# Optimization experiments

Hardware: AMD Instinct MI355X
Metric: run time of the kernel (lower is better)

The kernel has to match this reference:

```python
import jax, jax.numpy as jnp
import numpy as np


def setup_inputs() -> dict:
    key = jax.random.key(0)
    ks = jax.random.split(key, 5)
    B, S, D, F = 4, 2048, 1024, 4096
    scale_w1 = 1.0 / np.sqrt(D)
    scale_w2 = 1.0 / np.sqrt(F)
    return {
        "hidden_states": jax.random.normal(ks[0], (B, S, D), dtype=jnp.float32),
        "W1": jax.random.normal(ks[1], (F, D), dtype=jnp.float32) * scale_w1,
        "b1": jax.random.normal(ks[2], (F,), dtype=jnp.float32) * 0.02,
        "W2": jax.random.normal(ks[3], (D, F), dtype=jnp.float32) * scale_w2,
        "b2": jax.random.normal(ks[4], (D,), dtype=jnp.float32) * 0.02,
    }


def _sigmoid_poly(h):
    # cubic polynomial sigmoid approximation: 0.5 + 0.25*h - 0.0208*h^3
    h2 = h * h
    h3 = h2 * h
    return 0.5 + 0.25 * h + (-0.0208) * h3


def reference(hidden_states, W1, b1, W2, b2):
    # secure linear projection == plain affine: x @ W.T + b
    h = jnp.einsum("bsd,fd->bsf", hidden_states, W1) + b1  # [B,S,F]
    sw = h * _sigmoid_poly(h)                               # swish via poly sigmoid
    out = jnp.einsum("bsf,df->bsd", sw, W2) + b2            # [B,S,D]
    return out
```

## Files before the change

kernel.cpp:

```cpp
#include <hip/hip_runtime.h>
#include <hip/hip_bf16.h>

typedef __bf16 bf16_t;
typedef __bf16 bf16x8 __attribute__((ext_vector_type(8)));
typedef float f32x16 __attribute__((ext_vector_type(16)));

__global__ __launch_bounds__(256) void cast3_f32_to_bf16(
    const float* __restrict__ a, bf16_t* __restrict__ ao, int na8,
    const float* __restrict__ b, bf16_t* __restrict__ bo, int nb8,
    const float* __restrict__ c, bf16_t* __restrict__ co, int nc8) {
  int i = blockIdx.x * blockDim.x + threadIdx.x;
  const float* in;
  bf16_t* out;
  int j;
  if (i < na8) {
    in = a; out = ao; j = i;
  } else if (i < na8 + nb8) {
    in = b; out = bo; j = i - na8;
  } else if (i < na8 + nb8 + nc8) {
    in = c; out = co; j = i - na8 - nb8;
  } else {
    return;
  }
  const float4* in4 = (const float4*)in;
  float4 f0 = in4[2 * j];
  float4 f1 = in4[2 * j + 1];
  bf16x8 o;
  o[0] = (bf16_t)f0.x; o[1] = (bf16_t)f0.y;
  o[2] = (bf16_t)f0.z; o[3] = (bf16_t)f0.w;
  o[4] = (bf16_t)f1.x; o[5] = (bf16_t)f1.y;
  o[6] = (bf16_t)f1.z; o[7] = (bf16_t)f1.w;
  ((bf16x8*)out)[j] = o;
}

__device__ __forceinline__ void gload_lds16(const bf16_t* g, bf16_t* l) {
  __builtin_amdgcn_global_load_lds(
      (const __attribute__((address_space(1))) void*)g,
      (__attribute__((address_space(3))) void*)l,
      16, 0, 0);
}

template <bool SWISH>
__global__ __launch_bounds__(256, 2) void gemm_bt(
    const bf16_t* __restrict__ A, const bf16_t* __restrict__ B,
    const float* __restrict__ bias, void* __restrict__ Cout,
    int M, int N, int K, int XW, int px, int py) {
  const int tid = threadIdx.x;
  const int wave = tid >> 6;
  const int lane = tid & 63;

  const int bid = blockIdx.x;
  const int xcd = bid & 7;
  const int idx = bid >> 3;
  const int cx = xcd % XW;
  const int cy = xcd / XW;
  const int bx = cx * px + idx % px;
  const int by = cy * py + idx / px;
  const int tileM = by << 8;
  const int tileN = bx << 7;

  __shared__ __align__(16) bf16_t sA[256 * 64];
  __shared__ __align__(16) bf16_t sB[128 * 64];

  const int lrow = lane >> 3;
  const int gch = ((lane & 7) ^ lrow) << 3;
  const bf16_t* gA = A + (size_t)(tileM + (wave << 6) + lrow) * K + gch;
  const bf16_t* gB = B + (size_t)(tileN + (wave << 5) + lrow) * K + gch;
  bf16_t* lA = sA + (size_t)(wave << 6) * 64;
  bf16_t* lB = sB + (size_t)(wave << 5) * 64;

  const int wr = wave >> 1, wc = wave & 1;
  const int frow = lane & 31;
  const int p0 = (((lane >> 5) ^ (lane & 7)) << 3);
  int offA[4], offB[2];
#pragma unroll
  for (int i = 0; i < 4; ++i)
    offA[i] = (wr * 128 + i * 32 + frow) * 64 + p0;
#pragma unroll
  for (int j = 0; j < 2; ++j)
    offB[j] = (wc * 64 + j * 32 + frow) * 64 + p0;

  f32x16 acc[4][2] = {};

  for (int kt = 0; kt < K; kt += 64) {
#pragma unroll
    for (int r = 0; r < 8; ++r)
      gload_lds16(gA + kt + (size_t)(r * 8) * K, lA + r * 8 * 64);
#pragma unroll
    for (int r = 0; r < 4; ++r)
      gload_lds16(gB + kt + (size_t)(r * 8) * K, lB + r * 8 * 64);
    __syncthreads();

#pragma unroll
    for (int s = 0; s < 4; ++s) {
      const int sx = s << 4;
      bf16x8 af[4], bg[2];
#pragma unroll
      for (int i = 0; i < 4; ++i)
        af[i] = *(const bf16x8*)(sA + (offA[i] ^ sx));
#pragma unroll
      for (int j = 0; j < 2; ++j)
        bg[j] = *(const bf16x8*)(sB + (offB[j] ^ sx));
#pragma unroll
      for (int i = 0; i < 4; ++i)
#pragma unroll
        for (int j = 0; j < 2; ++j)
          acc[i][j] = __builtin_amdgcn_mfma_f32_32x32x16_bf16(
              af[i], bg[j], acc[i][j], 0, 0, 0);
    }
    __syncthreads();
  }

  const int halfsel = (lane >> 5) << 2;
#pragma unroll
  for (int i = 0; i < 4; ++i) {
    const int row0 = tileM + wr * 128 + i * 32 + halfsel;
#pragma unroll
    for (int j = 0; j < 2; ++j) {
      const int col = tileN + wc * 64 + j * 32 + (lane & 31);
      const float bv = bias[col];
#pragma unroll
      for (int r = 0; r < 16; ++r) {
        const int row = row0 + (r & 3) + ((r >> 2) << 3);
        float h = acc[i][j][r] + bv;
        if constexpr (SWISH) {
          float h3 = h * h * h;
          float sw = h * (0.5f + 0.25f * h - 0.0208f * h3);
          ((bf16_t*)Cout)[(size_t)row * N + col] = (bf16_t)sw;
        } else {
          ((float*)Cout)[(size_t)row * N + col] = h;
        }
      }
    }
  }
}

extern "C" void kernel_launch(void* const* d_in, const int* in_sizes, int n_in,
                              void* d_out, int out_size, void* d_ws,
                              size_t ws_size, hipStream_t stream) {
  const float* X  = (const float*)d_in[0];
  const float* W1 = (const float*)d_in[1];
  const float* b1 = (const float*)d_in[2];
  const float* W2 = (const float*)d_in[3];
  const float* b2 = (const float*)d_in[4];
  float* out = (float*)d_out;

  const int F = in_sizes[2];
  const int D = in_sizes[4];
  const int M = in_sizes[0] / D;

  bf16_t* Xb  = (bf16_t*)d_ws;
  bf16_t* W1b = Xb + (size_t)M * D;
  bf16_t* W2b = W1b + (size_t)F * D;
  bf16_t* SW  = W2b + (size_t)D * F;

  const int nX = (M * D) / 8, nW1 = (F * D) / 8, nW2 = (D * F) / 8;
  const int nTot = nX + nW1 + nW2;
  cast3_f32_to_bf16<<<(nTot + 255) / 256, 256, 0, stream>>>(
      X, Xb, nX, W1, W1b, nW1, W2, W2b, nW2);

  {
    const int gx = F / 128, gy = M / 256;
    const int XW = 2, XH = 4;
    const int px = gx / XW, py = gy / XH;
    gemm_bt<true><<<gx * gy, 256, 0, stream>>>(
        Xb, W1b, b1, (void*)SW, M, F, D, XW, px, py);
  }

  {
    const int gx = D / 128, gy = M / 256;
    const int XW = 1, XH = 8;
    const int px = gx / XW, py = gy / XH;
    gemm_bt<false><<<gx * gy, 256, 0, stream>>>(
        SW, W2b, b2, (void*)out, M, D, F, XW, px, py);
  }
}
```

Before: 272.0 us.

## Shrink GEMM tile to 128x128 and prefetch next K-tile via registers

Replaces direct global-to-LDS loads with register-staged loads that fetch the next K-slice while MFMAs run on the current one, then write it to LDS after a barrier. The M tile shrinks from 256 to 128, halving the accumulators per wave and doubling the grid. The aim is to hide global load latency and raise occupancy. The cost is extra VGPRs for staging, an extra barrier per iteration, and lower data reuse per tile, which raises global and L2 traffic.

Measured after the change: 268.4 us. No clear change (-1.3%).

```diff
diff --git a/kernel.cpp b/kernel.cpp
--- a/kernel.cpp
+++ b/kernel.cpp
@@ -33,13 +33,6 @@
   ((bf16x8*)out)[j] = o;
 }
 
-__device__ __forceinline__ void gload_lds16(const bf16_t* g, bf16_t* l) {
-  __builtin_amdgcn_global_load_lds(
-      (const __attribute__((address_space(1))) void*)g,
-      (__attribute__((address_space(3))) void*)l,
-      16, 0, 0);
-}
-
 template <bool SWISH>
 __global__ __launch_bounds__(256, 2) void gemm_bt(
     const bf16_t* __restrict__ A, const bf16_t* __restrict__ B,
@@ -56,65 +49,83 @@
   const int cy = xcd / XW;
   const int bx = cx * px + idx % px;
   const int by = cy * py + idx / px;
-  const int tileM = by << 8;
+  const int tileM = by << 7;
   const int tileN = bx << 7;
 
-  __shared__ __align__(16) bf16_t sA[256 * 64];
+  __shared__ __align__(16) bf16_t sA[128 * 64];
   __shared__ __align__(16) bf16_t sB[128 * 64];
 
   const int lrow = lane >> 3;
   const int gch = ((lane & 7) ^ lrow) << 3;
-  const bf16_t* gA = A + (size_t)(tileM + (wave << 6) + lrow) * K + gch;
+  const bf16_t* gA = A + (size_t)(tileM + (wave << 5) + lrow) * K + gch;
   const bf16_t* gB = B + (size_t)(tileN + (wave << 5) + lrow) * K + gch;
-  bf16_t* lA = sA + (size_t)(wave << 6) * 64;
-  bf16_t* lB = sB + (size_t)(wave << 5) * 64;
+  bf16_t* wAp = sA + (size_t)(wave << 5) * 64 + (lane << 3);
+  bf16_t* wBp = sB + (size_t)(wave << 5) * 64 + (lane << 3);
 
   const int wr = wave >> 1, wc = wave & 1;
   const int frow = lane & 31;
   const int p0 = (((lane >> 5) ^ (lane & 7)) << 3);
-  int offA[4], offB[2];
+  int offA[2], offB[2];
 #pragma unroll
-  for (int i = 0; i < 4; ++i)
-    offA[i] = (wr * 128 + i * 32 + frow) * 64 + p0;
+  for (int i = 0; i < 2; ++i)
+    offA[i] = (wr * 64 + i * 32 + frow) * 64 + p0;
 #pragma unroll
   for (int j = 0; j < 2; ++j)
     offB[j] = (wc * 64 + j * 32 + frow) * 64 + p0;
 
-  f32x16 acc[4][2] = {};
+  f32x16 acc[2][2] = {};
 
-  for (int kt = 0; kt < K; kt += 64) {
+  const int niter = K >> 6;
+
+  bf16x8 vA[4], vB[4];
 #pragma unroll
-    for (int r = 0; r < 8; ++r)
-      gload_lds16(gA + kt + (size_t)(r * 8) * K, lA + r * 8 * 64);
+  for (int r = 0; r < 4; ++r) {
+    vA[r] = *(const bf16x8*)(gA + (size_t)(r * 8) * K);
+    vB[r] = *(const bf16x8*)(gB + (size_t)(r * 8) * K);
+  }
 #pragma unroll
-    for (int r = 0; r < 4; ++r)
-      gload_lds16(gB + kt + (size_t)(r * 8) * K, lB + r * 8 * 64);
-    __syncthreads();
+  for (int r = 0; r < 4; ++r) {
+    *(bf16x8*)(wAp + r * 512) = vA[r];
+    *(bf16x8*)(wBp + r * 512) = vB[r];
+  }
+  __syncthreads();
 
+  for (int it = 0; it < niter; ++it) {
+    if (it + 1 < niter) {
+      const int kt = (it + 1) << 6;
+#pragma unroll
+      for (int r = 0; r < 4; ++r) {
+        vA[r] = *(const bf16x8*)(gA + kt + (size_t)(r * 8) * K);
+        vB[r] = *(const bf16x8*)(gB + kt + (size_t)(r * 8) * K);
+      }
+    }
 #pragma unroll
     for (int s = 0; s < 4; ++s) {
       const int sx = s << 4;
-      bf16x8 af[4], bg[2];
+      bf16x8 a0 = *(const bf16x8*)(sA + (offA[0] ^ sx));
+      bf16x8 a1 = *(const bf16x8*)(sA + (offA[1] ^ sx));
+      bf16x8 b0 = *(const bf16x8*)(sB + (offB[0] ^ sx));
+      bf16x8 b1 = *(const bf16x8*)(sB + (offB[1] ^ sx));
+      acc[0][0] = __builtin_amdgcn_mfma_f32_32x32x16_bf16(a0, b0, acc[0][0], 0, 0, 0);
+      acc[0][1] = __builtin_amdgcn_mfma_f32_32x32x16_bf16(a0, b1, acc[0][1], 0, 0, 0);
+      acc[1][0] = __builtin_amdgcn_mfma_f32_32x32x16_bf16(a1, b0, acc[1][0], 0, 0, 0);
+      acc[1][1] = __builtin_amdgcn_mfma_f32_32x32x16_bf16(a1, b1, acc[1][1], 0, 0, 0);
+    }
+    __syncthreads();
+    if (it + 1 < niter) {
 #pragma unroll
-      for (int i = 0; i < 4; ++i)
-        af[i] = *(const bf16x8*)(sA + (offA[i] ^ sx));
-#pragma unroll
-      for (int j = 0; j < 2; ++j)
-        bg[j] = *(const bf16x8*)(sB + (offB[j] ^ sx));
-#pragma unroll
-      for (int i = 0; i < 4; ++i)
-#pragma unroll
-        for (int j = 0; j < 2; ++j)
-          acc[i][j] = __builtin_amdgcn_mfma_f32_32x32x16_bf16(
-              af[i], bg[j], acc[i][j], 0, 0, 0);
+      for (int r = 0; r < 4; ++r) {
+        *(bf16x8*)(wAp + r * 512) = vA[r];
+        *(bf16x8*)(wBp + r * 512) = vB[r];
+      }
     }
     __syncthreads();
   }
 
   const int halfsel = (lane >> 5) << 2;
 #pragma unroll
-  for (int i = 0; i < 4; ++i) {
-    const int row0 = tileM + wr * 128 + i * 32 + halfsel;
+  for (int i = 0; i < 2; ++i) {
+    const int row0 = tileM + wr * 64 + i * 32 + halfsel;
 #pragma unroll
     for (int j = 0; j < 2; ++j) {
       const int col = tileN + wc * 64 + j * 32 + (lane & 31);
@@ -160,7 +171,7 @@
       X, Xb, nX, W1, W1b, nW1, W2, W2b, nW2);
 
   {
-    const int gx = F / 128, gy = M / 256;
+    const int gx = F / 128, gy = M / 128;
     const int XW = 2, XH = 4;
     const int px = gx / XW, py = gy / XH;
     gemm_bt<true><<<gx * gy, 256, 0, stream>>>(
@@ -168,7 +179,7 @@
   }
 
   {
-    const int gx = D / 128, gy = M / 256;
+    const int gx = D / 128, gy = M / 128;
     const int XW = 1, XH = 8;
     const int px = gx / XW, py = gy / XH;
     gemm_bt<false><<<gx * gy, 256, 0, stream>>>(
```

## Double-buffer GEMM tiles via register staging instead of direct global-to-LDS loads

Applied to the files above, without the earlier changes.

Replaces the direct global_load_lds path with loads into registers that are later written into a double-buffered shared-memory tile. The next k-tile is fetched while the current one is computed, so global latency overlaps with the MFMA work. This doubles LDS use, adds 24 bf16x8 staging registers per thread, and lowers the launch bound to one block per CU, which reduces occupancy. It also adds explicit LDS store instructions that the old direct-to-LDS loads avoided.

Result: slower. 280.0 us (+2.9%).

```diff
diff --git a/kernel.cpp b/kernel.cpp
--- a/kernel.cpp
+++ b/kernel.cpp
@@ -33,15 +33,44 @@
   ((bf16x8*)out)[j] = o;
 }
 
-__device__ __forceinline__ void gload_lds16(const bf16_t* g, bf16_t* l) {
-  __builtin_amdgcn_global_load_lds(
-      (const __attribute__((address_space(1))) void*)g,
-      (__attribute__((address_space(3))) void*)l,
-      16, 0, 0);
-}
+#define STAGE_LOAD(SET, KT)                                          \
+  {                                                                  \
+    const int kt_ = (KT);                                            \
+    _Pragma("unroll") for (int r = 0; r < 8; ++r)                    \
+        SET[r] = *(const bf16x8*)(gA + kt_ + (size_t)(r * 8) * K);   \
+    _Pragma("unroll") for (int r = 0; r < 4; ++r)                    \
+        SET[8 + r] = *(const bf16x8*)(gB + kt_ + (size_t)(r * 8) * K); \
+  }
+
+#define STAGE_WRITE(SET, BUFSEL)                                        \
+  {                                                                     \
+    _Pragma("unroll") for (int r = 0; r < 8; ++r)                       \
+        *(bf16x8*)(sA + (BUFSEL) * (256 * 64) + wAoff + r * 512) = SET[r]; \
+    _Pragma("unroll") for (int r = 0; r < 4; ++r)                       \
+        *(bf16x8*)(sB + (BUFSEL) * (128 * 64) + wBoff + r * 512) =      \
+            SET[8 + r];                                                 \
+  }
+
+#define COMPUTE(BUFSEL)                                                 \
+  {                                                                     \
+    const bf16_t* bA = sA + (BUFSEL) * (256 * 64);                      \
+    const bf16_t* bB = sB + (BUFSEL) * (128 * 64);                      \
+    _Pragma("unroll") for (int s = 0; s < 4; ++s) {                     \
+      const int sx = s << 4;                                            \
+      bf16x8 af[4], bg[2];                                              \
+      _Pragma("unroll") for (int i = 0; i < 4; ++i)                     \
+          af[i] = *(const bf16x8*)(bA + (offA[i] ^ sx));                \
+      _Pragma("unroll") for (int j = 0; j < 2; ++j)                     \
+          bg[j] = *(const bf16x8*)(bB + (offB[j] ^ sx));                \
+      _Pragma("unroll") for (int i = 0; i < 4; ++i)                     \
+          _Pragma("unroll") for (int j = 0; j < 2; ++j)                 \
+              acc[i][j] = __builtin_amdgcn_mfma_f32_32x32x16_bf16(      \
+                  af[i], bg[j], acc[i][j], 0, 0, 0);                    \
+    }                                                                   \
+  }
 
 template <bool SWISH>
-__global__ __launch_bounds__(256, 2) void gemm_bt(
+__global__ __launch_bounds__(256, 1) void gemm_bt(
     const bf16_t* __restrict__ A, const bf16_t* __restrict__ B,
     const float* __restrict__ bias, void* __restrict__ Cout,
     int M, int N, int K, int XW, int px, int py) {
@@ -59,15 +88,15 @@
   const int tileM = by << 8;
   const int tileN = bx << 7;
 
-  __shared__ __align__(16) bf16_t sA[256 * 64];
-  __shared__ __align__(16) bf16_t sB[128 * 64];
+  __shared__ __align__(16) bf16_t sA[2 * 256 * 64];
+  __shared__ __align__(16) bf16_t sB[2 * 128 * 64];
 
   const int lrow = lane >> 3;
   const int gch = ((lane & 7) ^ lrow) << 3;
   const bf16_t* gA = A + (size_t)(tileM + (wave << 6) + lrow) * K + gch;
   const bf16_t* gB = B + (size_t)(tileN + (wave << 5) + lrow) * K + gch;
-  bf16_t* lA = sA + (size_t)(wave << 6) * 64;
-  bf16_t* lB = sB + (size_t)(wave << 5) * 64;
+  const int wAoff = ((wave << 6) + lrow) * 64 + ((lane & 7) << 3);
+  const int wBoff = ((wave << 5) + lrow) * 64 + ((lane & 7) << 3);
 
   const int wr = wave >> 1, wc = wave & 1;
   const int frow = lane & 31;
@@ -82,32 +111,22 @@
 
   f32x16 acc[4][2] = {};
 
-  for (int kt = 0; kt < K; kt += 64) {
-#pragma unroll
-    for (int r = 0; r < 8; ++r)
-      gload_lds16(gA + kt + (size_t)(r * 8) * K, lA + r * 8 * 64);
-#pragma unroll
-    for (int r = 0; r < 4; ++r)
-      gload_lds16(gB + kt + (size_t)(r * 8) * K, lB + r * 8 * 64);
+  const int niter = K >> 6;
+
+  bf16x8 S0[12], S1[12];
+  STAGE_LOAD(S0, 0);
+  STAGE_WRITE(S0, 0);
+  STAGE_LOAD(S1, 64);
+  __syncthreads();
+
+  for (int j = 0; j < niter; j += 2) {
+    if (j + 2 < niter) STAGE_LOAD(S0, (j + 2) << 6);
+    COMPUTE(0);
+    STAGE_WRITE(S1, 1);
     __syncthreads();
-
-#pragma unroll
-    for (int s = 0; s < 4; ++s) {
-      const int sx = s << 4;
-      bf16x8 af[4], bg[2];
-#pragma unroll
-      for (int i = 0; i < 4; ++i)
-        af[i] = *(const bf16x8*)(sA + (offA[i] ^ sx));
-#pragma unroll
-      for (int j = 0; j < 2; ++j)
-        bg[j] = *(const bf16x8*)(sB + (offB[j] ^ sx));
-#pragma unroll
-      for (int i = 0; i < 4; ++i)
-#pragma unroll
-        for (int j = 0; j < 2; ++j)
-          acc[i][j] = __builtin_amdgcn_mfma_f32_32x32x16_bf16(
-              af[i], bg[j], acc[i][j], 0, 0, 0);
-    }
+    if (j + 3 < niter) STAGE_LOAD(S1, (j + 3) << 6);
+    COMPUTE(1);
+    if (j + 2 < niter) STAGE_WRITE(S0, 0);
     __syncthreads();
   }
 
@@ -175,3 +194,7 @@
         SW, W2b, b2, (void*)out, M, D, F, XW, px, py);
   }
 }
+
+#undef STAGE_LOAD
+#undef STAGE_WRITE
+#undef COMPUTE
```
